# Performance work log

Measured on AMD Instinct MI355X. Metric: run time of the kernel, lower is better.

## Reference

```python
import jax, jax.numpy as jnp
import numpy as np
from jax import lax

H = 2048      # d_inner
N = 8         # half of d_state (conjugate-pair complex modes)
B, L, D_MODEL = 4, 4096, 1024
D_CONV = 4


def setup_inputs() -> dict:
    key = jax.random.key(0)
    ks = jax.random.split(key, 10)
    hidden_states = jax.random.normal(ks[0], (B, L, D_MODEL), dtype=jnp.float32)
    W_in = jax.random.normal(ks[1], (2 * H, D_MODEL), dtype=jnp.float32) / np.sqrt(D_MODEL)
    conv_w = jax.random.normal(ks[2], (H, D_CONV), dtype=jnp.float32) / np.sqrt(D_CONV)
    conv_b = jax.random.normal(ks[3], (H,), dtype=jnp.float32) * 0.1
    # S4D params: dt ~ loguniform(1e-3, 1e-1); A = -0.5 + i*pi*n (legs-ish diag init)
    u = jax.random.uniform(ks[4], (H,), dtype=jnp.float32)
    log_dt = jnp.log(1e-3) + u * (jnp.log(1e-1) - jnp.log(1e-3))
    log_A_real = jnp.log(0.5 * jnp.ones((H, N), dtype=jnp.float32))
    A_imag = jnp.pi * jnp.broadcast_to(jnp.arange(N, dtype=jnp.float32), (H, N)).copy()
    C_re = jax.random.normal(ks[5], (H, N), dtype=jnp.float32)
    C_im = jax.random.normal(ks[6], (H, N), dtype=jnp.float32)
    D = jnp.ones((H,), dtype=jnp.float32)
    W_out = jax.random.normal(ks[7], (D_MODEL, H), dtype=jnp.float32) / np.sqrt(H)
    return dict(hidden_states=hidden_states, W_in=W_in, conv_w=conv_w, conv_b=conv_b,
                log_dt=log_dt, log_A_real=log_A_real, A_imag=A_imag,
                C_re=C_re, C_im=C_im, D=D, W_out=W_out)


def _s4d_kernel(log_dt, log_A_real, A_imag, C_re, C_im, L):
    # S4D (diagonal SSM) convolution kernel, ZOH-style discretization.
    dt = jnp.exp(log_dt)                       # (H,)
    A = -jnp.exp(log_A_real) + 1j * A_imag      # (H,N) complex
    C = C_re + 1j * C_im                        # (H,N)
    dtA = dt[:, None] * A                       # (H,N)
    Ct = C * (jnp.exp(dtA) - 1.0) / A           # (H,N)
    t = jnp.arange(L, dtype=jnp.float32)
    vand = jnp.exp(dtA[:, :, None] * t)         # (H,N,L) Vandermonde
    return 2.0 * jnp.einsum('hn,hnl->hl', Ct, vand).real  # (H,L)


def reference(hidden_states, W_in, conv_w, conv_b, log_dt, log_A_real, A_imag, C_re, C_im, D, W_out):
    B, L, _ = hidden_states.shape
    # in_proj (no bias): (B,L,D) -> (B, 2H, L)
    xz = jnp.einsum('bld,ed->bel', hidden_states, W_in)
    x, z = jnp.split(xz, 2, axis=1)             # each (B,H,L)
    # causal depthwise conv1d + SiLU
    w = conv_w.shape[-1]
    xp = jnp.pad(x, ((0, 0), (0, 0), (w - 1, 0)))
    x = lax.conv_general_dilated(xp, conv_w[:, None, :], (1,), 'VALID',
                                 dimension_numbers=('NCH', 'OIH', 'NCH'),
                                 feature_group_count=x.shape[1])
    x = jax.nn.silu(x + conv_b[None, :, None])
    # S4 FFT long convolution + D skip
    k = _s4d_kernel(log_dt, log_A_real, A_imag, C_re, C_im, L)  # (H,L)
    n = 2 * L
    y = jnp.fft.irfft(jnp.fft.rfft(x, n=n) * jnp.fft.rfft(k, n=n), n=n)[..., :L]
    y = y + x * D[None, :, None]
    # SiLU gate and out_proj
    y = y * jax.nn.silu(z)
    return jnp.einsum('bhl,dh->bld', y, W_out)
```

## Files before the change

kernel.cpp:

```cpp
#include <hip/hip_runtime.h>
#include <hip/hip_bf16.h>
#include <math.h>

#define H_DIM 2048
#define N_ST 8
#define B_SZ 4
#define L_SEQ 4096
#define DMODEL 1024
#define DCONV 4
#define CL 128
#define NC (L_SEQ / CL)

typedef __bf16 bf16x8 __attribute__((ext_vector_type(8)));
typedef __bf16 bf16x4 __attribute__((ext_vector_type(4)));
typedef float f32x4 __attribute__((ext_vector_type(4)));

typedef const unsigned int __attribute__((address_space(1)))* gptr_t;
typedef unsigned int __attribute__((address_space(3)))* lptr_t;

__device__ __forceinline__ void gl_lds16(const __bf16* g, __bf16* l) {
    __builtin_amdgcn_global_load_lds((gptr_t)g, (lptr_t)l, 16, 0, 0);
}

#define WS_XZ     0
#define WS_YTH    8388608
#define WS_YTL    12582912
#define WS_COEF   16777216
#define WS_STATES 16875520
#define WS_LOOK   17924096
#define WS_HH     18186240
#define WS_HL     20283392
#define WS_WIH    22380544
#define WS_WIL    24477696
#define WS_WOH    26574848
#define WS_WOL    27623424

__global__ __launch_bounds__(256) void cvt_split4(const float* __restrict__ s,
                                                  __bf16* __restrict__ h,
                                                  __bf16* __restrict__ l, int n4) {
    int i = blockIdx.x * 256 + threadIdx.x;
    if (i >= n4) return;
    float4 v = ((const float4*)s)[i];
    float vv[4] = {v.x, v.y, v.z, v.w};
    bf16x4 hv, lv;
#pragma unroll
    for (int j = 0; j < 4; ++j) {
        __bf16 hb = (__bf16)vv[j];
        hv[j] = hb;
        lv[j] = (__bf16)(vv[j] - (float)hb);
    }
    *(bf16x4*)&h[(size_t)i * 4] = hv;
    *(bf16x4*)&l[(size_t)i * 4] = lv;
}

__global__ void coef_kernel(const float* __restrict__ log_dt,
                            const float* __restrict__ log_A_real,
                            const float* __restrict__ A_imag,
                            const float* __restrict__ C_re,
                            const float* __restrict__ C_im,
                            float* __restrict__ coef) {
    int i = blockIdx.x * blockDim.x + threadIdx.x;
    if (i >= H_DIM * N_ST) return;
    int h = i >> 3;
    float dt = expf(log_dt[h]);
    float Ar = -expf(log_A_real[i]);
    float Ai = A_imag[i];
    float er = expf(dt * Ar);
    float ang = dt * Ai;
    float wr = er * cosf(ang);
    float wi = er * sinf(ang);
    float den = Ar * Ar + Ai * Ai;
    float qr = ((wr - 1.f) * Ar + wi * Ai) / den;
    float qi = (wi * Ar - (wr - 1.f) * Ai) / den;
    float Cr = C_re[i], Ci = C_im[i];
    float Ctr = Cr * qr - Ci * qi;
    float Cti = Cr * qi + Ci * qr;
    float eCL = expf((float)CL * dt * Ar);
    float aCL = (float)CL * dt * Ai;
    float pr = eCL * cosf(aCL);
    float pi = eCL * sinf(aCL);
    const int HN = H_DIM * N_ST;
    coef[i]          = wr;
    coef[HN + i]     = wi;
    coef[2 * HN + i] = Ctr;
    coef[3 * HN + i] = Cti;
    coef[4 * HN + i] = pr;
    coef[5 * HN + i] = pi;
}

__global__ __launch_bounds__(256, 2) void gemm_split(const __bf16* __restrict__ Ah,
                                                     const __bf16* __restrict__ Al,
                                                     const __bf16* __restrict__ Bh,
                                                     const __bf16* __restrict__ Bl,
                                                     float* __restrict__ C,
                                                     int K, int ldc) {
    __shared__ __bf16 sAh[4096], sAl[4096], sBh[4096], sBl[4096];
    const int tid = threadIdx.x;
    const int lane = tid & 63;
    const int wid = tid >> 6;
    const int wr = wid >> 1, wc = wid & 1;
    const int bm = blockIdx.y, bn = blockIdx.x;

    const int r = tid & 127;
    const int kbq = tid >> 7;
    const size_t arow = (size_t)(bm * 128 + r) * K;
    const size_t brow = (size_t)(bn * 128 + r) * K;

    f32x4 acc[4][4];
#pragma unroll
    for (int m = 0; m < 4; ++m)
#pragma unroll
        for (int n = 0; n < 4; ++n) acc[m][n] = (f32x4){0.f, 0.f, 0.f, 0.f};

    const int kb = lane >> 4, rr = lane & 15;

    for (int k0 = 0; k0 < K; k0 += 32) {
        __syncthreads();
#pragma unroll
        for (int q = 0; q < 2; ++q) {
            const int skb = q * 2 + kbq;
            const int lo = q * 2048 + tid * 8;
            const size_t go = k0 + skb * 8;
            gl_lds16(Ah + arow + go, &sAh[lo]);
            gl_lds16(Al + arow + go, &sAl[lo]);
            gl_lds16(Bh + brow + go, &sBh[lo]);
            gl_lds16(Bl + brow + go, &sBl[lo]);
        }
        __syncthreads();

        bf16x8 fAh[4], fAl[4], fBh[4], fBl[4];
#pragma unroll
        for (int m = 0; m < 4; ++m) {
            int off = kb * 1024 + (wr * 64 + m * 16 + rr) * 8;
            fAh[m] = *(const bf16x8*)&sAh[off];
            fAl[m] = *(const bf16x8*)&sAl[off];
        }
#pragma unroll
        for (int n = 0; n < 4; ++n) {
            int off = kb * 1024 + (wc * 64 + n * 16 + rr) * 8;
            fBh[n] = *(const bf16x8*)&sBh[off];
            fBl[n] = *(const bf16x8*)&sBl[off];
        }
#pragma unroll
        for (int m = 0; m < 4; ++m)
#pragma unroll
            for (int n = 0; n < 4; ++n) {
                acc[m][n] = __builtin_amdgcn_mfma_f32_16x16x32_bf16(fAh[m], fBh[n], acc[m][n], 0, 0, 0);
                acc[m][n] = __builtin_amdgcn_mfma_f32_16x16x32_bf16(fAh[m], fBl[n], acc[m][n], 0, 0, 0);
                acc[m][n] = __builtin_amdgcn_mfma_f32_16x16x32_bf16(fAl[m], fBh[n], acc[m][n], 0, 0, 0);
            }
    }

    const int rq = lane >> 4;
#pragma unroll
    for (int m = 0; m < 4; ++m)
#pragma unroll
        for (int n = 0; n < 4; ++n) {
            int col = bn * 128 + wc * 64 + n * 16 + rr;
            int row0 = bm * 128 + wr * 64 + m * 16 + rq * 4;
#pragma unroll
            for (int j = 0; j < 4; ++j)
                C[(size_t)(row0 + j) * ldc + col] = acc[m][n][j];
        }
}

__global__ __launch_bounds__(256) void scan_phase1(const float* __restrict__ xz,
                                                   const float* __restrict__ coef,
                                                   const float* __restrict__ conv_w,
                                                   const float* __restrict__ conv_b,
                                                   float* __restrict__ states,
                                                   float* __restrict__ look) {
    int t = blockIdx.x * 256 + threadIdx.x;
    int c = t & (NC - 1);
    int h = t >> 5;

    const int HN = H_DIM * N_ST;
    float wr[N_ST], wi[N_ST];
#pragma unroll
    for (int n = 0; n < N_ST; ++n) {
        wr[n] = coef[h * N_ST + n];
        wi[n] = coef[HN + h * N_ST + n];
    }
    float cw0 = conv_w[h * 4 + 0], cw1 = conv_w[h * 4 + 1];
    float cw2 = conv_w[h * 4 + 2], cw3 = conv_w[h * 4 + 3];
    float cb = conv_b[h];

    const float* xrow = xz + (size_t)h * L_SEQ + c * CL;
    float x3 = 0.f, x2 = 0.f, x1 = 0.f;
    if (c > 0) {
        float4 p = *(const float4*)(xrow - 4);
        x3 = p.y; x2 = p.z; x1 = p.w;
    }
    *(float4*)(look + (size_t)t * 4) = make_float4(x3, x2, x1, 0.f);

    float sr[N_ST], si[N_ST];
#pragma unroll
    for (int n = 0; n < N_ST; ++n) { sr[n] = 0.f; si[n] = 0.f; }

    for (int j = 0; j < CL; j += 4) {
        float4 v = *(const float4*)(xrow + j);
        float xv[4] = {v.x, v.y, v.z, v.w};
#pragma unroll
        for (int k = 0; k < 4; ++k) {
            float u = cw0 * x3 + cw1 * x2 + cw2 * x1 + cw3 * xv[k] + cb;
            float xc = u / (1.f + __expf(-u));
            x3 = x2; x2 = x1; x1 = xv[k];
#pragma unroll
            for (int n = 0; n < N_ST; ++n) {
                float nr = wr[n] * sr[n] - wi[n] * si[n] + xc;
                float ni = wr[n] * si[n] + wi[n] * sr[n];
                sr[n] = nr; si[n] = ni;
            }
        }
    }
    float* st = states + (size_t)t * (N_ST * 2);
#pragma unroll
    for (int n = 0; n < N_ST; ++n) { st[2 * n] = sr[n]; st[2 * n + 1] = si[n]; }
}

__global__ __launch_bounds__(256) void scan_phase2(const float* __restrict__ coef,
                                                   float* __restrict__ states) {
    int h = blockIdx.x * 256 + threadIdx.x;
    if (h >= H_DIM) return;
    const int HN = H_DIM * N_ST;
    float pr[N_ST], pi[N_ST];
#pragma unroll
    for (int n = 0; n < N_ST; ++n) {
        pr[n] = coef[4 * HN + h * N_ST + n];
        pi[n] = coef[5 * HN + h * N_ST + n];
    }
    float sr[N_ST], si[N_ST];
#pragma unroll
    for (int n = 0; n < N_ST; ++n) { sr[n] = 0.f; si[n] = 0.f; }
    float* base = states + (size_t)h * NC * (N_ST * 2);
    for (int c = 0; c < NC; ++c) {
        float* st = base + c * (N_ST * 2);
#pragma unroll
        for (int n = 0; n < N_ST; ++n) {
            float lr = st[2 * n], li = st[2 * n + 1];
            st[2 * n] = sr[n]; st[2 * n + 1] = si[n];
            float nr = pr[n] * sr[n] - pi[n] * si[n] + lr;
            float ni = pr[n] * si[n] + pi[n] * sr[n] + li;
            sr[n] = nr; si[n] = ni;
        }
    }
}

__global__ __launch_bounds__(256) void scan_phase3(float* __restrict__ xz,
                                                   const float* __restrict__ coef,
                                                   const float* __restrict__ conv_w,
                                                   const float* __restrict__ conv_b,
                                                   const float* __restrict__ Dvec,
                                                   const float* __restrict__ states,
                                                   const float* __restrict__ look) {
    int t = blockIdx.x * 256 + threadIdx.x;
    int c = t & (NC - 1);
    int h = t >> 5;

    const int HN = H_DIM * N_ST;
    float wr[N_ST], wi[N_ST], Ctr[N_ST], Cti[N_ST];
#pragma unroll
    for (int n = 0; n < N_ST; ++n) {
        wr[n]  = coef[h * N_ST + n];
        wi[n]  = coef[HN + h * N_ST + n];
        Ctr[n] = coef[2 * HN + h * N_ST + n];
        Cti[n] = coef[3 * HN + h * N_ST + n];
    }
    float cw0 = conv_w[h * 4 + 0], cw1 = conv_w[h * 4 + 1];
    float cw2 = conv_w[h * 4 + 2], cw3 = conv_w[h * 4 + 3];
    float cb = conv_b[h];
    float Dh = Dvec[h];

    float* xrow = xz + (size_t)h * L_SEQ + c * CL;
    const float* zrow = xz + (size_t)(H_DIM + h) * L_SEQ + c * CL;

    float4 lk = *(const float4*)(look + (size_t)t * 4);
    float x3 = lk.x, x2 = lk.y, x1 = lk.z;

    const float* st = states + (size_t)t * (N_ST * 2);
    float sr[N_ST], si[N_ST];
#pragma unroll
    for (int n = 0; n < N_ST; ++n) { sr[n] = st[2 * n]; si[n] = st[2 * n + 1]; }

    for (int j = 0; j < CL; j += 4) {
        float4 v = *(const float4*)(xrow + j);
        float4 zv = *(const float4*)(zrow + j);
        float xv[4] = {v.x, v.y, v.z, v.w};
        float zz[4] = {zv.x, zv.y, zv.z, zv.w};
        float out[4];
#pragma unroll
        for (int k = 0; k < 4; ++k) {
            float u = cw0 * x3 + cw1 * x2 + cw2 * x1 + cw3 * xv[k] + cb;
            float xc = u / (1.f + __expf(-u));
            x3 = x2; x2 = x1; x1 = xv[k];
            float accy = 0.f;
#pragma unroll
            for (int n = 0; n < N_ST; ++n) {
                float nr = wr[n] * sr[n] - wi[n] * si[n] + xc;
                float ni = wr[n] * si[n] + wi[n] * sr[n];
                sr[n] = nr; si[n] = ni;
                accy += Ctr[n] * nr - Cti[n] * ni;
            }
            float yv = 2.f * accy + Dh * xc;
            float g = zz[k] / (1.f + __expf(-zz[k]));
            out[k] = yv * g;
        }
        *(float4*)(xrow + j) = make_float4(out[0], out[1], out[2], out[3]);
    }
}

__global__ __launch_bounds__(256) void transpose_split(const float* __restrict__ y,
                                                       __bf16* __restrict__ th,
                                                       __bf16* __restrict__ tl) {
    __shared__ float tile[64][65];
    const int l0 = blockIdx.x * 64, h0 = blockIdx.y * 64;
    const int tid = threadIdx.x;
    const int r = tid >> 4, c4 = (tid & 15) * 4;
#pragma unroll
    for (int p = 0; p < 4; ++p) {
        float4 v = *(const float4*)(y + (size_t)(h0 + r + p * 16) * L_SEQ + l0 + c4);
        tile[r + p * 16][c4 + 0] = v.x;
        tile[r + p * 16][c4 + 1] = v.y;
        tile[r + p * 16][c4 + 2] = v.z;
        tile[r + p * 16][c4 + 3] = v.w;
    }
    __syncthreads();
    const int l = tid >> 2, hb = (tid & 3) * 16;
    float vals[16];
#pragma unroll
    for (int j = 0; j < 16; ++j) vals[j] = tile[hb + j][l];
    bf16x8 hv0, hv1, lv0, lv1;
#pragma unroll
    for (int j = 0; j < 8; ++j) {
        __bf16 hbv = (__bf16)vals[j];
        hv0[j] = hbv;
        lv0[j] = (__bf16)(vals[j] - (float)hbv);
        __bf16 hbv2 = (__bf16)vals[j + 8];
        hv1[j] = hbv2;
        lv1[j] = (__bf16)(vals[j + 8] - (float)hbv2);
    }
    size_t base = (size_t)(l0 + l) * H_DIM + h0 + hb;
    *(bf16x8*)&th[base] = hv0;
    *(bf16x8*)&th[base + 8] = hv1;
    *(bf16x8*)&tl[base] = lv0;
    *(bf16x8*)&tl[base + 8] = lv1;
}

extern "C" void kernel_launch(void* const* d_in, const int* in_sizes, int n_in,
                              void* d_out, int out_size, void* d_ws, size_t ws_size,
                              hipStream_t stream) {
    const float* hid        = (const float*)d_in[0];
    const float* W_in       = (const float*)d_in[1];
    const float* conv_w     = (const float*)d_in[2];
    const float* conv_b     = (const float*)d_in[3];
    const float* log_dt     = (const float*)d_in[4];
    const float* log_A_real = (const float*)d_in[5];
    const float* A_imag     = (const float*)d_in[6];
    const float* C_re       = (const float*)d_in[7];
    const float* C_im       = (const float*)d_in[8];
    const float* Dv         = (const float*)d_in[9];
    const float* W_out      = (const float*)d_in[10];
    float* out = (float*)d_out;
    float* ws  = (float*)d_ws;

    float* xz      = ws + WS_XZ;
    __bf16* yTh    = (__bf16*)(ws + WS_YTH);
    __bf16* yTl    = (__bf16*)(ws + WS_YTL);
    float* coef    = ws + WS_COEF;
    float* states  = ws + WS_STATES;
    float* look    = ws + WS_LOOK;
    __bf16* Hh     = (__bf16*)(ws + WS_HH);
    __bf16* Hl     = (__bf16*)(ws + WS_HL);
    __bf16* Wih    = (__bf16*)(ws + WS_WIH);
    __bf16* Wil    = (__bf16*)(ws + WS_WIL);
    __bf16* Woh    = (__bf16*)(ws + WS_WOH);
    __bf16* Wol    = (__bf16*)(ws + WS_WOL);

    coef_kernel<<<(H_DIM * N_ST + 255) / 256, 256, 0, stream>>>(
        log_dt, log_A_real, A_imag, C_re, C_im, coef);

    cvt_split4<<<(2 * H_DIM * DMODEL / 4 + 255) / 256, 256, 0, stream>>>(W_in, Wih, Wil, 2 * H_DIM * DMODEL / 4);
    cvt_split4<<<(DMODEL * H_DIM / 4 + 255) / 256, 256, 0, stream>>>(W_out, Woh, Wol, DMODEL * H_DIM / 4);

    const int nscan = H_DIM * NC;
    dim3 gIn(L_SEQ / 128, 2 * H_DIM / 128);
    dim3 gOut(DMODEL / 128, L_SEQ / 128);
    dim3 gTr(L_SEQ / 64, H_DIM / 64);

    for (int b = 0; b < B_SZ; ++b) {
        const float* hid_b = hid + (size_t)b * L_SEQ * DMODEL;
        float* out_b = out + (size_t)b * L_SEQ * DMODEL;

        cvt_split4<<<(L_SEQ * DMODEL / 4 + 255) / 256, 256, 0, stream>>>(hid_b, Hh, Hl, L_SEQ * DMODEL / 4);
        gemm_split<<<gIn, 256, 0, stream>>>(Wih, Wil, Hh, Hl, xz, DMODEL, L_SEQ);
        scan_phase1<<<nscan / 256, 256, 0, stream>>>(xz, coef, conv_w, conv_b, states, look);
        scan_phase2<<<(H_DIM + 255) / 256, 256, 0, stream>>>(coef, states);
        scan_phase3<<<nscan / 256, 256, 0, stream>>>(xz, coef, conv_w, conv_b, Dv, states, look);
        transpose_split<<<gTr, 256, 0, stream>>>(xz, yTh, yTl);
        gemm_split<<<gOut, 256, 0, stream>>>(yTh, yTl, Woh, Wol, out_b, H_DIM, DMODEL);
    }
}
```

Baseline: 1.689 ms.

## Double-buffer LDS in split-bf16 GEMM and remap blocks across XCDs

The split-precision GEMM now keeps two LDS stages and prefetches the tile two K-steps ahead with global_load_lds. Explicit vmcnt/lgkmcnt waits plus barriers replace the old per-iteration __syncthreads pair, so global loads overlap MFMA work. The 2D grid becomes a 1D grid with a swizzle that groups consecutive tiles onto the same XCD (bid&7 striping), aiming for better L2 reuse. LDS use doubles to 64KB per block, which may limit the occupancy the launch bounds ask for.

```diff
diff --git a/kernel.cpp b/kernel.cpp
--- a/kernel.cpp
+++ b/kernel.cpp
@@ -93,16 +93,20 @@
                                                      const __bf16* __restrict__ Bh,
                                                      const __bf16* __restrict__ Bl,
                                                      float* __restrict__ C,
-                                                     int K, int ldc) {
-    __shared__ __bf16 sAh[4096], sAl[4096], sBh[4096], sBl[4096];
+                                                     int K, int ldc, int gx) {
+    __shared__ __bf16 sAh[2][4096], sAl[2][4096], sBh[2][4096], sBl[2][4096];
     const int tid = threadIdx.x;
     const int lane = tid & 63;
     const int wid = tid >> 6;
-    const int wr = wid >> 1, wc = wid & 1;
-    const int bm = blockIdx.y, bn = blockIdx.x;
+    const int wrw = wid >> 1, wcw = wid & 1;
+
+    const int nwg = gridDim.x;
+    const int bid = blockIdx.x;
+    const int swz = (bid & 7) * (nwg >> 3) + (bid >> 3);
+    const int bn = swz % gx, bm = swz / gx;
 
     const int r = tid & 127;
-    const int kbq = tid >> 7;
+    const int kbq8 = (tid >> 7) * 8;
     const size_t arow = (size_t)(bm * 128 + r) * K;
     const size_t brow = (size_t)(bn * 128 + r) * K;
 
@@ -114,32 +118,40 @@
 
     const int kb = lane >> 4, rr = lane & 15;
 
-    for (int k0 = 0; k0 < K; k0 += 32) {
-        __syncthreads();
+    auto stage = [&](int b, int k0) {
 #pragma unroll
         for (int q = 0; q < 2; ++q) {
-            const int skb = q * 2 + kbq;
             const int lo = q * 2048 + tid * 8;
-            const size_t go = k0 + skb * 8;
-            gl_lds16(Ah + arow + go, &sAh[lo]);
-            gl_lds16(Al + arow + go, &sAl[lo]);
-            gl_lds16(Bh + brow + go, &sBh[lo]);
-            gl_lds16(Bl + brow + go, &sBl[lo]);
-        }
-        __syncthreads();
+            const size_t go = (size_t)k0 + q * 16 + kbq8;
+            gl_lds16(Ah + arow + go, &sAh[b][lo]);
+            gl_lds16(Al + arow + go, &sAl[b][lo]);
+            gl_lds16(Bh + brow + go, &sBh[b][lo]);
+            gl_lds16(Bl + brow + go, &sBl[b][lo]);
+        }
+    };
+
+    const int nt = K >> 5;
+    stage(0, 0);
+    stage(1, 32);
+
+    for (int t = 0; t < nt; ++t) {
+        const int cur = t & 1;
+        if (t < nt - 1) asm volatile("s_waitcnt vmcnt(8)" ::: "memory");
+        else            asm volatile("s_waitcnt vmcnt(0)" ::: "memory");
+        __builtin_amdgcn_s_barrier();
 
         bf16x8 fAh[4], fAl[4], fBh[4], fBl[4];
 #pragma unroll
         for (int m = 0; m < 4; ++m) {
-            int off = kb * 1024 + (wr * 64 + m * 16 + rr) * 8;
-            fAh[m] = *(const bf16x8*)&sAh[off];
-            fAl[m] = *(const bf16x8*)&sAl[off];
+            int off = kb * 1024 + (wrw * 64 + m * 16 + rr) * 8;
+            fAh[m] = *(const bf16x8*)&sAh[cur][off];
+            fAl[m] = *(const bf16x8*)&sAl[cur][off];
         }
 #pragma unroll
         for (int n = 0; n < 4; ++n) {
-            int off = kb * 1024 + (wc * 64 + n * 16 + rr) * 8;
-            fBh[n] = *(const bf16x8*)&sBh[off];
-            fBl[n] = *(const bf16x8*)&sBl[off];
+            int off = kb * 1024 + (wcw * 64 + n * 16 + rr) * 8;
+            fBh[n] = *(const bf16x8*)&sBh[cur][off];
+            fBl[n] = *(const bf16x8*)&sBl[cur][off];
         }
 #pragma unroll
         for (int m = 0; m < 4; ++m)
@@ -149,6 +161,10 @@
                 acc[m][n] = __builtin_amdgcn_mfma_f32_16x16x32_bf16(fAh[m], fBl[n], acc[m][n], 0, 0, 0);
                 acc[m][n] = __builtin_amdgcn_mfma_f32_16x16x32_bf16(fAl[m], fBh[n], acc[m][n], 0, 0, 0);
             }
+
+        asm volatile("s_waitcnt lgkmcnt(0)" ::: "memory");
+        __builtin_amdgcn_s_barrier();
+        if (t + 2 < nt) stage(cur, (t + 2) << 5);
     }
 
     const int rq = lane >> 4;
@@ -156,8 +172,8 @@
     for (int m = 0; m < 4; ++m)
 #pragma unroll
         for (int n = 0; n < 4; ++n) {
-            int col = bn * 128 + wc * 64 + n * 16 + rr;
-            int row0 = bm * 128 + wr * 64 + m * 16 + rq * 4;
+            int col = bn * 128 + wcw * 64 + n * 16 + rr;
+            int row0 = bm * 128 + wrw * 64 + m * 16 + rq * 4;
 #pragma unroll
             for (int j = 0; j < 4; ++j)
                 C[(size_t)(row0 + j) * ldc + col] = acc[m][n][j];
@@ -383,8 +399,8 @@
     cvt_split4<<<(DMODEL * H_DIM / 4 + 255) / 256, 256, 0, stream>>>(W_out, Woh, Wol, DMODEL * H_DIM / 4);
 
     const int nscan = H_DIM * NC;
-    dim3 gIn(L_SEQ / 128, 2 * H_DIM / 128);
-    dim3 gOut(DMODEL / 128, L_SEQ / 128);
+    const int nwgIn  = (L_SEQ / 128) * (2 * H_DIM / 128);
+    const int nwgOut = (DMODEL / 128) * (L_SEQ / 128);
     dim3 gTr(L_SEQ / 64, H_DIM / 64);
 
     for (int b = 0; b < B_SZ; ++b) {
@@ -392,11 +408,11 @@
         float* out_b = out + (size_t)b * L_SEQ * DMODEL;
 
         cvt_split4<<<(L_SEQ * DMODEL / 4 + 255) / 256, 256, 0, stream>>>(hid_b, Hh, Hl, L_SEQ * DMODEL / 4);
-        gemm_split<<<gIn, 256, 0, stream>>>(Wih, Wil, Hh, Hl, xz, DMODEL, L_SEQ);
+        gemm_split<<<nwgIn, 256, 0, stream>>>(Wih, Wil, Hh, Hl, xz, DMODEL, L_SEQ, L_SEQ / 128);
         scan_phase1<<<nscan / 256, 256, 0, stream>>>(xz, coef, conv_w, conv_b, states, look);
         scan_phase2<<<(H_DIM + 255) / 256, 256, 0, stream>>>(coef, states);
         scan_phase3<<<nscan / 256, 256, 0, stream>>>(xz, coef, conv_w, conv_b, Dv, states, look);
         transpose_split<<<gTr, 256, 0, stream>>>(xz, yTh, yTl);
-        gemm_split<<<gOut, 256, 0, stream>>>(yTh, yTl, Woh, Wol, out_b, H_DIM, DMODEL);
-    }
-}
+        gemm_split<<<nwgOut, 256, 0, stream>>>(yTh, yTl, Woh, Wol, out_b, H_DIM, DMODEL, DMODEL / 128);
+    }
+}
```

Measured after the change: 1.707 ms. No clear change (+1.1%).
